# Kernel optimization log

Measured on AMD Instinct MI355X. Metric: run time of the kernel, lower is better.

Reference implementation:

```python
import jax, jax.numpy as jnp
import numpy as np

EPS = 1e-5
EMBED_DIM = 1024
CTX_DIM = 768
NUM_HEADS = 16
DH = EMBED_DIM // NUM_HEADS
# Faithful to torch source: embed_dim // num_heads ** 0.5 parses as embed_dim // (num_heads**0.5)
SCALE = EMBED_DIM // (NUM_HEADS ** 0.5)  # = 256.0


def ws_conv1x1(x, w, b, mask):
    # weight-standardized 1x1 conv1d: w [O, I, 1], x [B, I, T]
    w2 = w[..., 0]
    mu = jnp.mean(w2, axis=1, keepdims=True)
    var = jnp.var(w2, axis=1, keepdims=True)
    wn = (w2 - mu) * jax.lax.rsqrt(var + EPS)
    y = jnp.einsum('oi,bit->bot', wn, x) + b[None, :, None]
    if mask is not None:
        y = jnp.where(mask, y, 0.0)  # mask [B,1,T] bool
    return y


def layernorm(x, g, b):
    # normalize over last axis
    mu = jnp.mean(x, axis=-1, keepdims=True)
    var = jnp.var(x, axis=-1, keepdims=True)
    return (x - mu) * jax.lax.rsqrt(var + EPS) * g + b


def setup_inputs() -> dict:
    key = jax.random.key(0)
    ks = jax.random.split(key, 16)
    B, T, S = 4, 1024, 1024
    inp = {
        'x': jax.random.normal(ks[0], (B, EMBED_DIM, T), dtype=jnp.float32),
        'context': jax.random.normal(ks[1], (B, CTX_DIM, S), dtype=jnp.float32),
        'mask': jax.random.randint(ks[2], (B, 1, T), 0, 2).astype(bool),
        'mask_ctx': jax.random.randint(ks[3], (B, 1, S), 0, 2).astype(bool),
        'qw': jax.random.normal(ks[4], (EMBED_DIM, EMBED_DIM, 1), dtype=jnp.float32) * 0.02,
        'qb': jnp.zeros((EMBED_DIM,), jnp.float32),
        'kw': jax.random.normal(ks[5], (EMBED_DIM, CTX_DIM, 1), dtype=jnp.float32) * 0.02,
        'kb': jnp.zeros((EMBED_DIM,), jnp.float32),
        'vw': jax.random.normal(ks[6], (EMBED_DIM, CTX_DIM, 1), dtype=jnp.float32) * 0.02,
        'vb': jnp.zeros((EMBED_DIM,), jnp.float32),
        'ow': jax.random.normal(ks[7], (EMBED_DIM, EMBED_DIM, 1), dtype=jnp.float32) * 0.02,
        'ob': jnp.zeros((EMBED_DIM,), jnp.float32),
        'gq': jnp.ones((DH,), jnp.float32), 'bq': jnp.zeros((DH,), jnp.float32),
        'gk': jnp.ones((DH,), jnp.float32), 'bk': jnp.zeros((DH,), jnp.float32),
        'gv': jnp.ones((DH,), jnp.float32), 'bv': jnp.zeros((DH,), jnp.float32),
    }
    return inp


def reference(x, context, mask, mask_ctx, qw, qb, kw, kb, vw, vb, ow, ob, gq, bq, gk, bk, gv, bv):
    B, E, T = x.shape
    S = context.shape[-1]
    q = ws_conv1x1(x, qw, qb, mask)            # [B,E,T]
    k = ws_conv1x1(context, kw, kb, mask_ctx)  # [B,E,S]
    v = ws_conv1x1(context, vw, vb, mask_ctx)  # [B,E,S]
    # split heads -> [B,H,dh,L]
    q = q.reshape(B, NUM_HEADS, DH, T)
    k = k.reshape(B, NUM_HEADS, DH, S)
    v = v.reshape(B, NUM_HEADS, DH, S)
    # middle_norm: LayerNorm over dh (applied on transposed layout)
    q = jnp.swapaxes(layernorm(jnp.swapaxes(q, -1, -2), gq, bq), -1, -2)
    k = jnp.swapaxes(layernorm(jnp.swapaxes(k, -1, -2), gk, bk), -1, -2)
    v = jnp.swapaxes(layernorm(jnp.swapaxes(v, -1, -2), gv, bv), -1, -2)
    # scores: k^T @ q -> [B,H,S,T]
    scores = jnp.einsum('bhds,bhdt->bhst', k, q) / SCALE
    scores = jnp.where(mask[:, :, None, :], scores, -1e9)  # mask over query dim T
    scores = jax.nn.softmax(scores, axis=-1)               # softmax over T (as in source)
    scores = jnp.where(mask_ctx[:, :, :, None], scores, 0.0)
    out = jnp.einsum('bhds,bhst->bhdt', v, scores)          # v @ scores -> [B,H,dh,T]
    out = out.reshape(B, E, T)
    out = ws_conv1x1(out, ow, ob, mask) + x
    return out
```

## Files before the change

### kernel.cpp

```cpp
#include <hip/hip_runtime.h>

#define NB 4
#define TT 1024
#define SS 1024
#define EE 1024
#define CCH 768
#define NH 16
#define DHH 64
#define EPSF 1e-5f
#define QSCALE (1.4426950408889634f / 256.0f)

typedef unsigned short u16;
typedef __attribute__((ext_vector_type(8))) short short8;
typedef __attribute__((ext_vector_type(8))) unsigned short u16x8;
typedef __attribute__((ext_vector_type(4))) unsigned short u16x4;
typedef __attribute__((ext_vector_type(4))) float f32x4;

__device__ __forceinline__ u16 f2bu(float f) {
    union { float f; unsigned u; } x; x.f = f;
    unsigned r = x.u + 0x7fffu + ((x.u >> 16) & 1u);
    return (u16)(r >> 16);
}
__device__ __forceinline__ float bu2f(u16 u) {
    union { unsigned u; float f; } x; x.u = ((unsigned)u) << 16; return x.f;
}

#if __has_builtin(__builtin_amdgcn_exp2f)
#define EXP2(x) __builtin_amdgcn_exp2f(x)
#else
#define EXP2(x) exp2f(x)
#endif

#define MFMA16(a, b, c) __builtin_amdgcn_mfma_f32_16x16x32_bf16((a), (b), (c), 0, 0, 0)

__global__ __launch_bounds__(256) void mask_scan(
    const int* __restrict__ mask, const int* __restrict__ mask_ctx,
    int* __restrict__ posQ, int* __restrict__ posK,
    int* __restrict__ tIdx, int* __restrict__ sIdx,
    int* __restrict__ cntQ, int* __restrict__ cntK) {
    int which = blockIdx.x & 1, b = blockIdx.x >> 1;
    const int* m = (which ? mask_ctx : mask) + b * 1024;
    int* pos = (which ? posK : posQ) + b * 1024;
    int* idx = (which ? sIdx : tIdx) + b * 1024;
    int* cnt = (which ? cntK : cntQ) + b;
    int tid = threadIdx.x;
    int base = tid * 4;
    int v[4]; int s = 0;
#pragma unroll
    for (int i = 0; i < 4; i++) { v[i] = m[base + i] ? 1 : 0; s += v[i]; }
    int lane = tid & 63, wid = tid >> 6;
    int inc = s;
#pragma unroll
    for (int off = 1; off < 64; off <<= 1) {
        int o = __shfl_up(inc, off);
        if (lane >= off) inc += o;
    }
    __shared__ int wtot[4];
    if (lane == 63) wtot[wid] = inc;
    __syncthreads();
    int woff = 0;
    for (int i = 0; i < wid; i++) woff += wtot[i];
    int p = woff + inc - s;
#pragma unroll
    for (int i = 0; i < 4; i++) {
        pos[base + i] = p;
        if (v[i]) idx[p] = base + i;
        p += v[i];
    }
    if (tid == 255) *cnt = p;
}

__global__ __launch_bounds__(256) void ws_norm4(
    const float* __restrict__ qw, const float* __restrict__ kw,
    const float* __restrict__ vw, const float* __restrict__ ow,
    u16* __restrict__ wqn, u16* __restrict__ wkn,
    u16* __restrict__ wvn, u16* __restrict__ won) {
    int mat = blockIdx.y;
    const float* w = mat == 0 ? qw : (mat == 1 ? kw : (mat == 2 ? vw : ow));
    u16* wn = mat == 0 ? wqn : (mat == 1 ? wkn : (mat == 2 ? wvn : won));
    int I = (mat == 1 || mat == 2) ? CCH : EE;
    int row = blockIdx.x;
    const float* wr = w + (size_t)row * I;
    float s = 0.f, s2 = 0.f;
    for (int i = threadIdx.x; i < I; i += 256) { float v = wr[i]; s += v; s2 += v * v; }
#pragma unroll
    for (int off = 32; off > 0; off >>= 1) { s += __shfl_down(s, off); s2 += __shfl_down(s2, off); }
    __shared__ float sa[4], sb[4], smean, srstd;
    int wid = threadIdx.x >> 6;
    if ((threadIdx.x & 63) == 0) { sa[wid] = s; sb[wid] = s2; }
    __syncthreads();
    if (threadIdx.x == 0) {
        float ts = sa[0] + sa[1] + sa[2] + sa[3];
        float ts2 = sb[0] + sb[1] + sb[2] + sb[3];
        float mean = ts / (float)I;
        float var = ts2 / (float)I - mean * mean;
        smean = mean; srstd = rsqrtf(var + EPSF);
    }
    __syncthreads();
    float mean = smean, r = srstd;
    u16* wo = wn + (size_t)row * I;
    for (int i = threadIdx.x; i < I; i += 256) wo[i] = f2bu((wr[i] - mean) * r);
}

__global__ __launch_bounds__(256) void transpose2_f2b(
    const float* __restrict__ x, const float* __restrict__ ctx,
    u16* __restrict__ xT, u16* __restrict__ cT) {
    __shared__ float tile[64][65];
    int yy = blockIdx.y;
    int mat = yy < 16 ? 0 : 1;
    int r0 = (mat == 0 ? yy : yy - 16) * 64;
    int R = mat == 0 ? EE : CCH;
    const float* in = mat == 0 ? x : ctx;
    u16* out = mat == 0 ? xT : cT;
    int c0 = blockIdx.x * 64, b = blockIdx.z;
    const float* ip = in + (size_t)b * R * 1024;
    u16* op = out + (size_t)b * R * 1024;
    int tid = threadIdx.x;
#pragma unroll
    for (int m = 0; m < 16; m++) {
        int id = tid + 256 * m; int r = id >> 6, c = id & 63;
        tile[r][c] = ip[(size_t)(r0 + r) * 1024 + c0 + c];
    }
    __syncthreads();
#pragma unroll
    for (int m = 0; m < 16; m++) {
        int id = tid + 256 * m; int rr = id >> 6, cc = id & 63;
        op[(size_t)(c0 + rr) * R + r0 + cc] = f2bu(tile[cc][rr]);
    }
}

__device__ __forceinline__ void gemm_core(
    const u16* __restrict__ A, const u16* __restrict__ Bp, int I,
    int o0, int l0, u16 (*at)[72], u16 (*bt)[72], f32x4 (&acc)[4][2]) {
    int tid = threadIdx.x;
    int w = tid >> 6, lane = tid & 63, quad = lane >> 4, l16 = lane & 15;
    int wm = w & 1, wn = w >> 1;
    int rA = tid >> 3, cA = (tid & 7) * 8;
    u16x8 ra[2][4], rb[2][2];
#pragma unroll
    for (int p = 0; p < 2; p++) {
        int kb = p * 64;
#pragma unroll
        for (int m = 0; m < 4; m++)
            ra[p][m] = *(const u16x8*)&A[(size_t)(o0 + rA + 32 * m) * I + kb + cA];
#pragma unroll
        for (int m = 0; m < 2; m++)
            rb[p][m] = *(const u16x8*)&Bp[(size_t)(l0 + rA + 32 * m) * I + kb + cA];
    }
    for (int k0 = 0; k0 < I; k0 += 128) {
#pragma unroll
        for (int half = 0; half < 2; half++) {
            __syncthreads();
#pragma unroll
            for (int m = 0; m < 4; m++) *(u16x8*)&at[rA + 32 * m][cA] = ra[half][m];
#pragma unroll
            for (int m = 0; m < 2; m++) *(u16x8*)&bt[rA + 32 * m][cA] = rb[half][m];
            __syncthreads();
            int kpre = k0 + half * 64 + 128;
            if (kpre < I) {
#pragma unroll
                for (int m = 0; m < 4; m++)
                    ra[half][m] = *(const u16x8*)&A[(size_t)(o0 + rA + 32 * m) * I + kpre + cA];
#pragma unroll
                for (int m = 0; m < 2; m++)
                    rb[half][m] = *(const u16x8*)&Bp[(size_t)(l0 + rA + 32 * m) * I + kpre + cA];
            }
#pragma unroll
            for (int ks = 0; ks < 64; ks += 32) {
                short8 af[4], bf[2];
#pragma unroll
                for (int i = 0; i < 4; i++)
                    af[i] = *(const short8*)&at[wm * 64 + i * 16 + l16][ks + quad * 8];
#pragma unroll
                for (int j = 0; j < 2; j++)
                    bf[j] = *(const short8*)&bt[wn * 32 + j * 16 + l16][ks + quad * 8];
#pragma unroll
                for (int mt = 0; mt < 4; mt++)
#pragma unroll
                    for (int nt = 0; nt < 2; nt++)
                        acc[mt][nt] = MFMA16(af[mt], bf[nt], acc[mt][nt]);
            }
        }
    }
}

__global__ __launch_bounds__(256) void proj_qkv(
    const u16* __restrict__ wq, const u16* __restrict__ wk, const u16* __restrict__ wv,
    const u16* __restrict__ xT, const u16* __restrict__ cT,
    const float* __restrict__ qb, const float* __restrict__ kb, const float* __restrict__ vbi,
    const int* __restrict__ mask_t, const int* __restrict__ mask_c,
    const int* __restrict__ posQ, const int* __restrict__ posK,
    const float* __restrict__ gq, const float* __restrict__ bq,
    const float* __restrict__ gk, const float* __restrict__ bk,
    u16* __restrict__ qc, u16* __restrict__ kc, u16* __restrict__ yv) {
    __shared__ u16 at[128][72];
    __shared__ u16 bt[64][72];
    __shared__ float sg[64], sbe[64], sbias[128];
    int tid = threadIdx.x;
    int w = tid >> 6, lane = tid & 63, quad = lane >> 4, l16 = lane & 15;
    int wm = w & 1, wn = w >> 1;
    int mat = blockIdx.y >> 3;
    int o0 = (blockIdx.y & 7) * 128;
    int l0 = blockIdx.x * 64;
    int b = blockIdx.z;
    const u16* A = mat == 0 ? wq : (mat == 1 ? wk : wv);
    const u16* BT = mat == 0 ? xT : cT;
    const float* bias = mat == 0 ? qb : (mat == 1 ? kb : vbi);
    const int* maskp = mat == 0 ? mask_t : mask_c;
    int I = mat == 0 ? EE : CCH;
    if (mat < 2 && tid < 64) {
        sg[tid] = (mat == 0 ? gq : gk)[tid];
        sbe[tid] = (mat == 0 ? bq : bk)[tid];
    }
    if (tid < 128) sbias[tid] = bias[o0 + tid];

    f32x4 acc[4][2] = {};
    gemm_core(A, BT + (size_t)b * 1024 * I, I, o0, l0, at, bt, acc);

    const int* mrow = maskp + (size_t)b * 1024;
    if (mat < 2) {
        u16* outT = mat == 0 ? qc : kc;
        const int* posArr = (mat == 0 ? posQ : posK) + (size_t)b * 1024;
        float scale = mat == 0 ? QSCALE : 1.0f;
        int h = (o0 >> 6) + wm;
        int bh = b * NH + h;
#pragma unroll
        for (int nt = 0; nt < 2; nt++) {
            int l = l0 + wn * 32 + nt * 16 + l16;
            int mval = mrow[l];
            float vbuf[16];
            float s = 0.f;
#pragma unroll
            for (int mt = 0; mt < 4; mt++)
#pragma unroll
                for (int reg = 0; reg < 4; reg++) {
                    float v = mval ? (acc[mt][nt][reg] + sbias[wm * 64 + mt * 16 + quad * 4 + reg]) : 0.f;
                    vbuf[mt * 4 + reg] = v; s += v;
                }
            s += __shfl_xor(s, 16); s += __shfl_xor(s, 32);
            float mean = s * (1.f / 64);
            float s2 = 0.f;
#pragma unroll
            for (int i = 0; i < 16; i++) { float dv = vbuf[i] - mean; s2 += dv * dv; }
            s2 += __shfl_xor(s2, 16); s2 += __shfl_xor(s2, 32);
            float r = rsqrtf(s2 * (1.f / 64) + EPSF);
            if (mval) {
                int pos = posArr[l];
                u16* op = outT + ((size_t)bh * 1024 + pos) * 64;
#pragma unroll
                for (int mt = 0; mt < 4; mt++) {
                    u16x4 pk;
#pragma unroll
                    for (int reg = 0; reg < 4; reg++) {
                        int d = mt * 16 + quad * 4 + reg;
                        pk[reg] = f2bu(((vbuf[mt * 4 + reg] - mean) * r * sg[d] + sbe[d]) * scale);
                    }
                    *(u16x4*)&op[mt * 16 + quad * 4] = pk;
                }
            }
        }
    } else {
#pragma unroll
        for (int nt = 0; nt < 2; nt++) {
            int l = l0 + wn * 32 + nt * 16 + l16;
            int mval = mrow[l];
#pragma unroll
            for (int mt = 0; mt < 4; mt++)
#pragma unroll
                for (int reg = 0; reg < 4; reg++) {
                    int o = o0 + wm * 64 + mt * 16 + quad * 4 + reg;
                    float v = mval ? (acc[mt][nt][reg] + sbias[wm * 64 + mt * 16 + quad * 4 + reg]) : 0.f;
                    yv[((size_t)b * EE + o) * 1024 + l] = f2bu(v);
                }
        }
    }
}

__global__ __launch_bounds__(256) void proj_o(
    const u16* __restrict__ won, const u16* __restrict__ aT,
    const float* __restrict__ obi, const int* __restrict__ mask,
    const float* __restrict__ x, float* __restrict__ out) {
    __shared__ u16 at[128][72];
    __shared__ u16 bt[64][72];
    __shared__ float sbias[128];
    int tid = threadIdx.x;
    int w = tid >> 6, lane = tid & 63, quad = lane >> 4, l16 = lane & 15;
    int wm = w & 1, wn = w >> 1;
    int o0 = blockIdx.y * 128, l0 = blockIdx.x * 64, b = blockIdx.z;
    if (tid < 128) sbias[tid] = obi[o0 + tid];
    f32x4 acc[4][2] = {};
    gemm_core(won, aT + (size_t)b * TT * EE, EE, o0, l0, at, bt, acc);
    const int* mrow = mask + (size_t)b * TT;
#pragma unroll
    for (int nt = 0; nt < 2; nt++) {
        int l = l0 + wn * 32 + nt * 16 + l16;
        int mval = mrow[l];
#pragma unroll
        for (int mt = 0; mt < 4; mt++)
#pragma unroll
            for (int reg = 0; reg < 4; reg++) {
                int o = o0 + wm * 64 + mt * 16 + quad * 4 + reg;
                float v = mval ? (acc[mt][nt][reg] + sbias[wm * 64 + mt * 16 + quad * 4 + reg]) : 0.f;
                size_t off = ((size_t)b * EE + o) * TT + l;
                out[off] = v + x[off];
            }
    }
}

__global__ __launch_bounds__(256) void attn_stats_mfma(
    const u16* __restrict__ qc, const u16* __restrict__ kc,
    const int* __restrict__ sIdx, const int* __restrict__ cntQ, const int* __restrict__ cntK,
    const float* __restrict__ gv, const float* __restrict__ bv,
    const u16* __restrict__ yv, u16* __restrict__ vc) {
    int s0 = blockIdx.x * 64, h = blockIdx.y, b = blockIdx.z;
    int Sc = cntK[b], Tc = cntQ[b];
    if (s0 >= Sc) return;
    __shared__ u16 kt[64][72];
    __shared__ u16 qt[64][72];
    __shared__ float lp[4][64];
    int tid = threadIdx.x;
    int w = tid >> 6, lane = tid & 63, quad = lane >> 4, l16 = lane & 15;
    int head = b * NH + h;
    const u16* kp = kc + (size_t)head * SS * DHH;
    const u16* qp = qc + (size_t)head * TT * DHH;
    int rA = tid >> 3, cA = (tid & 7) * 8;
#pragma unroll
    for (int m = 0; m < 2; m++)
        *(u16x8*)&kt[rA + 32 * m][cA] = *(const u16x8*)&kp[(size_t)(s0 + rA + 32 * m) * DHH + cA];
    u16x8 rq[2][2];
#pragma unroll
    for (int p = 0; p < 2; p++)
#pragma unroll
        for (int m = 0; m < 2; m++)
            rq[p][m] = *(const u16x8*)&qp[(size_t)(p * 64 + rA + 32 * m) * DHH + cA];
    float rl[4][4] = {};
    for (int t0 = 0; t0 < Tc; t0 += 128) {
#pragma unroll
        for (int half = 0; half < 2; half++) {
            int tb = t0 + half * 64;
            __syncthreads();
#pragma unroll
            for (int m = 0; m < 2; m++) *(u16x8*)&qt[rA + 32 * m][cA] = rq[half][m];
            __syncthreads();
            int tpre = tb + 128;
            if (tpre < TT) {
#pragma unroll
                for (int m = 0; m < 2; m++)
                    rq[half][m] = *(const u16x8*)&qp[(size_t)(tpre + rA + 32 * m) * DHH + cA];
            }
            int tcol = tb + w * 16 + l16;
            f32x4 acc[4] = {};
#pragma unroll
            for (int ks = 0; ks < 64; ks += 32) {
                short8 bf = *(const short8*)&qt[w * 16 + l16][ks + quad * 8];
#pragma unroll
                for (int mt = 0; mt < 4; mt++) {
                    short8 af = *(const short8*)&kt[mt * 16 + l16][ks + quad * 8];
                    acc[mt] = MFMA16(af, bf, acc[mt]);
                }
            }
            if (tcol < Tc) {
#pragma unroll
                for (int mt = 0; mt < 4; mt++)
#pragma unroll
                    for (int reg = 0; reg < 4; reg++)
                        rl[mt][reg] += EXP2(acc[mt][reg]);
            }
        }
    }
#pragma unroll
    for (int mt = 0; mt < 4; mt++) {
#pragma unroll
        for (int reg = 0; reg < 4; reg++) {
            float v = rl[mt][reg];
            v += __shfl_xor(v, 1); v += __shfl_xor(v, 2);
            v += __shfl_xor(v, 4); v += __shfl_xor(v, 8);
            if (l16 == 0) lp[w][mt * 16 + quad * 4 + reg] = v;
        }
    }
    __syncthreads();
    if (tid < 64 && s0 + tid < Sc) {
        int spos = s0 + tid;
        float lv = lp[0][tid] + lp[1][tid] + lp[2][tid] + lp[3][tid];
        float wsc = lv > 0.f ? (1.f / lv) : 0.f;
        int sreal = sIdx[(size_t)b * 1024 + spos];
        const u16* vin = yv + ((size_t)b * EE + h * 64) * SS + sreal;
        u16* vout = vc + ((size_t)b * EE + h * 64) * SS + spos;
        float sm = 0.f, s2 = 0.f;
        float vals[DHH];
#pragma unroll
        for (int d = 0; d < DHH; d++) {
            float v = bu2f(vin[(size_t)d * SS]);
            vals[d] = v; sm += v; s2 += v * v;
        }
        float mean = sm * (1.f / DHH);
        float var = s2 * (1.f / DHH) - mean * mean;
        float r = rsqrtf(var + EPSF);
#pragma unroll
        for (int d = 0; d < DHH; d++)
            vout[(size_t)d * SS] = f2bu(((vals[d] - mean) * r * gv[d] + bv[d]) * wsc);
    }
}

__global__ __launch_bounds__(256) void attn_pv_mfma(
    const u16* __restrict__ qc, const u16* __restrict__ kc, const u16* __restrict__ vc,
    const int* __restrict__ tIdx, const int* __restrict__ cntQ, const int* __restrict__ cntK,
    u16* __restrict__ aT) {
    int t0 = blockIdx.x * 64, h = blockIdx.y, b = blockIdx.z;
    int Tc = cntQ[b], Sc = cntK[b];
    if (t0 >= Tc) return;
    __shared__ u16 qt[64][72];
    __shared__ u16 kt[64][72];
    __shared__ u16 vt[64][72];
    __shared__ u16 pt[64][72];
    int tid = threadIdx.x;
    int w = tid >> 6, lane = tid & 63, quad = lane >> 4, l16 = lane & 15;
    int head = b * NH + h;
    const u16* qp = qc + (size_t)head * TT * DHH;
    const u16* kp = kc + (size_t)head * SS * DHH;
    const u16* vp = vc + ((size_t)head * DHH) * SS;
    int rA = tid >> 3, cA = (tid & 7) * 8;
#pragma unroll
    for (int m = 0; m < 2; m++)
        *(u16x8*)&qt[rA + 32 * m][cA] = *(const u16x8*)&qp[(size_t)(t0 + rA + 32 * m) * DHH + cA];
    u16x8 rk[2][2], rv[2][2];
#pragma unroll
    for (int p = 0; p < 2; p++)
#pragma unroll
        for (int m = 0; m < 2; m++) {
            rk[p][m] = *(const u16x8*)&kp[(size_t)(p * 64 + rA + 32 * m) * DHH + cA];
            rv[p][m] = *(const u16x8*)&vp[(size_t)(rA + 32 * m) * SS + p * 64 + cA];
        }
    int tl = w * 16 + l16;

    f32x4 oacc[4] = {};
    for (int s0 = 0; s0 < Sc; s0 += 128) {
#pragma unroll
        for (int half = 0; half < 2; half++) {
            int sb = s0 + half * 64;
            if (sb >= Sc) break;
            __syncthreads();
#pragma unroll
            for (int m = 0; m < 2; m++) {
                *(u16x8*)&kt[rA + 32 * m][cA] = rk[half][m];
                *(u16x8*)&vt[rA + 32 * m][cA] = rv[half][m];
            }
            __syncthreads();
            int spre = sb + 128;
            if (spre < SS) {
#pragma unroll
                for (int m = 0; m < 2; m++) {
                    rk[half][m] = *(const u16x8*)&kp[(size_t)(spre + rA + 32 * m) * DHH + cA];
                    rv[half][m] = *(const u16x8*)&vp[(size_t)(rA + 32 * m) * SS + spre + cA];
                }
            }
            f32x4 acc[4] = {};
#pragma unroll
            for (int ks = 0; ks < 64; ks += 32) {
                short8 bf = *(const short8*)&qt[tl][ks + quad * 8];
#pragma unroll
                for (int mt = 0; mt < 4; mt++) {
                    short8 af = *(const short8*)&kt[mt * 16 + l16][ks + quad * 8];
                    acc[mt] = MFMA16(af, bf, acc[mt]);
                }
            }
#pragma unroll
            for (int mt = 0; mt < 4; mt++) {
                u16x4 pk;
#pragma unroll
                for (int reg = 0; reg < 4; reg++) {
                    int sl = mt * 16 + quad * 4 + reg;
                    pk[reg] = (sb + sl < Sc) ? f2bu(EXP2(acc[mt][reg])) : (u16)0;
                }
                *(u16x4*)&pt[tl][mt * 16 + quad * 4] = pk;
            }
#pragma unroll
            for (int ks = 0; ks < 64; ks += 32) {
                short8 bf = *(const short8*)&pt[tl][ks + quad * 8];
#pragma unroll
                for (int mt = 0; mt < 4; mt++) {
                    short8 af = *(const short8*)&vt[mt * 16 + l16][ks + quad * 8];
                    oacc[mt] = MFMA16(af, bf, oacc[mt]);
                }
            }
        }
    }
    __syncthreads();
#pragma unroll
    for (int mt = 0; mt < 4; mt++) {
        u16x4 pk;
#pragma unroll
        for (int reg = 0; reg < 4; reg++) pk[reg] = f2bu(oacc[mt][reg]);
        *(u16x4*)&pt[tl][mt * 16 + quad * 4] = pk;
    }
    __syncthreads();
    const int* ti = tIdx + (size_t)b * 1024;
#pragma unroll
    for (int i = 0; i < 2; i++) {
        int id = tid * 2 + i;
        int r = id >> 3, c = (id & 7) * 8;
        if (t0 + r < Tc) {
            int treal = ti[t0 + r];
            *(u16x8*)&aT[((size_t)b * TT + treal) * EE + h * 64 + c] =
                *(const u16x8*)&pt[r][c];
        }
    }
}

extern "C" void kernel_launch(void* const* d_in, const int* in_sizes, int n_in,
                              void* d_out, int out_size, void* d_ws, size_t ws_size,
                              hipStream_t stream) {
    const float* x        = (const float*)d_in[0];
    const float* ctx      = (const float*)d_in[1];
    const int*   mask     = (const int*)d_in[2];
    const int*   mask_ctx = (const int*)d_in[3];
    const float* qw  = (const float*)d_in[4];
    const float* qbi = (const float*)d_in[5];
    const float* kw  = (const float*)d_in[6];
    const float* kbi = (const float*)d_in[7];
    const float* vw  = (const float*)d_in[8];
    const float* vbi = (const float*)d_in[9];
    const float* ow  = (const float*)d_in[10];
    const float* obi = (const float*)d_in[11];
    const float* gq = (const float*)d_in[12];
    const float* bq = (const float*)d_in[13];
    const float* gk = (const float*)d_in[14];
    const float* bk = (const float*)d_in[15];
    const float* gv = (const float*)d_in[16];
    const float* bv = (const float*)d_in[17];

    u16* p = (u16*)d_ws;
    u16* wqn = p; p += (size_t)EE * EE;
    u16* wkn = p; p += (size_t)EE * CCH;
    u16* wvn = p; p += (size_t)EE * CCH;
    u16* won = p; p += (size_t)EE * EE;
    u16* xT  = p; p += (size_t)NB * TT * EE;
    u16* cT  = p; p += (size_t)NB * SS * CCH;
    u16* yv  = p; p += (size_t)NB * EE * SS;
    u16* qc  = p; p += (size_t)NB * NH * TT * DHH;
    u16* kc  = p; p += (size_t)NB * NH * SS * DHH;
    u16* vc  = p; p += (size_t)NB * EE * SS;
    u16* aT  = p; p += (size_t)NB * TT * EE;
    int* posQ = (int*)p;
    int* posK = posQ + NB * 1024;
    int* tIdx = posK + NB * 1024;
    int* sIdx = tIdx + NB * 1024;
    int* cntQ = sIdx + NB * 1024;
    int* cntK = cntQ + NB;

    mask_scan<<<8, 256, 0, stream>>>(mask, mask_ctx, posQ, posK, tIdx, sIdx, cntQ, cntK);

    ws_norm4<<<dim3(1024, 4), 256, 0, stream>>>(qw, kw, vw, ow, wqn, wkn, wvn, won);

    transpose2_f2b<<<dim3(16, 28, NB), 256, 0, stream>>>(x, ctx, xT, cT);

    proj_qkv<<<dim3(16, 24, NB), 256, 0, stream>>>(
        wqn, wkn, wvn, xT, cT, qbi, kbi, vbi, mask, mask_ctx, posQ, posK,
        gq, bq, gk, bk, qc, kc, yv);

    attn_stats_mfma<<<dim3(16, NH, NB), 256, 0, stream>>>(
        qc, kc, sIdx, cntQ, cntK, gv, bv, yv, vc);

    attn_pv_mfma<<<dim3(16, NH, NB), 256, 0, stream>>>(
        qc, kc, vc, tIdx, cntQ, cntK, aT);

    proj_o<<<dim3(16, 8, NB), 256, 0, stream>>>(won, aT, obi, mask, x, (float*)d_out);
}
```

Baseline: 236.0 us.

## Compact masked tokens before QKV projection and skip fully masked GEMM tiles

The transpose kernel now runs its own prefix scan over the mask and writes only unmasked tokens, packed, into the bf16 transposed inputs. The QKV projection then exits early for tiles past the valid count, so it does roughly half the GEMM work. The separate mask-scan kernel is merged into the weight-standardization launch as an extra grid row, removing one launch. The trade-off is a redundant scan in every transpose block. Rows of the compacted buffers beyond the valid count are left unwritten, and downstream kernels are assumed to ignore them.

```diff
diff --git a/kernel.cpp b/kernel.cpp
--- a/kernel.cpp
+++ b/kernel.cpp
@@ -33,48 +33,46 @@
 
 #define MFMA16(a, b, c) __builtin_amdgcn_mfma_f32_16x16x32_bf16((a), (b), (c), 0, 0, 0)
 
-__global__ __launch_bounds__(256) void mask_scan(
-    const int* __restrict__ mask, const int* __restrict__ mask_ctx,
-    int* __restrict__ posQ, int* __restrict__ posK,
-    int* __restrict__ tIdx, int* __restrict__ sIdx,
-    int* __restrict__ cntQ, int* __restrict__ cntK) {
-    int which = blockIdx.x & 1, b = blockIdx.x >> 1;
-    const int* m = (which ? mask_ctx : mask) + b * 1024;
-    int* pos = (which ? posK : posQ) + b * 1024;
-    int* idx = (which ? sIdx : tIdx) + b * 1024;
-    int* cnt = (which ? cntK : cntQ) + b;
-    int tid = threadIdx.x;
-    int base = tid * 4;
-    int v[4]; int s = 0;
-#pragma unroll
-    for (int i = 0; i < 4; i++) { v[i] = m[base + i] ? 1 : 0; s += v[i]; }
-    int lane = tid & 63, wid = tid >> 6;
-    int inc = s;
-#pragma unroll
-    for (int off = 1; off < 64; off <<= 1) {
-        int o = __shfl_up(inc, off);
-        if (lane >= off) inc += o;
-    }
-    __shared__ int wtot[4];
-    if (lane == 63) wtot[wid] = inc;
-    __syncthreads();
-    int woff = 0;
-    for (int i = 0; i < wid; i++) woff += wtot[i];
-    int p = woff + inc - s;
-#pragma unroll
-    for (int i = 0; i < 4; i++) {
-        pos[base + i] = p;
-        if (v[i]) idx[p] = base + i;
-        p += v[i];
-    }
-    if (tid == 255) *cnt = p;
-}
-
-__global__ __launch_bounds__(256) void ws_norm4(
+__global__ __launch_bounds__(256) void ws_norm_scan(
     const float* __restrict__ qw, const float* __restrict__ kw,
     const float* __restrict__ vw, const float* __restrict__ ow,
     u16* __restrict__ wqn, u16* __restrict__ wkn,
-    u16* __restrict__ wvn, u16* __restrict__ won) {
+    u16* __restrict__ wvn, u16* __restrict__ won,
+    const int* __restrict__ mask, const int* __restrict__ mask_ctx,
+    int* __restrict__ tIdx, int* __restrict__ sIdx,
+    int* __restrict__ cntQ, int* __restrict__ cntK) {
+    int tid = threadIdx.x;
+    if (blockIdx.y == 4) {
+        if (blockIdx.x >= 8) return;
+        int which = blockIdx.x & 1, b = blockIdx.x >> 1;
+        const int* m = (which ? mask_ctx : mask) + b * 1024;
+        int* idx = (which ? sIdx : tIdx) + b * 1024;
+        int* cnt = (which ? cntK : cntQ) + b;
+        int base = tid * 4;
+        int v[4]; int s = 0;
+#pragma unroll
+        for (int i = 0; i < 4; i++) { v[i] = m[base + i] ? 1 : 0; s += v[i]; }
+        int lane = tid & 63, wid = tid >> 6;
+        int inc = s;
+#pragma unroll
+        for (int off = 1; off < 64; off <<= 1) {
+            int o = __shfl_up(inc, off);
+            if (lane >= off) inc += o;
+        }
+        __shared__ int wtot[4];
+        if (lane == 63) wtot[wid] = inc;
+        __syncthreads();
+        int woff = 0;
+        for (int i = 0; i < wid; i++) woff += wtot[i];
+        int p = woff + inc - s;
+#pragma unroll
+        for (int i = 0; i < 4; i++) {
+            if (v[i]) idx[p] = base + i;
+            p += v[i];
+        }
+        if (tid == 255) *cnt = p;
+        return;
+    }
     int mat = blockIdx.y;
     const float* w = mat == 0 ? qw : (mat == 1 ? kw : (mat == 2 ? vw : ow));
     u16* wn = mat == 0 ? wqn : (mat == 1 ? wkn : (mat == 2 ? wvn : won));
@@ -82,14 +80,14 @@
     int row = blockIdx.x;
     const float* wr = w + (size_t)row * I;
     float s = 0.f, s2 = 0.f;
-    for (int i = threadIdx.x; i < I; i += 256) { float v = wr[i]; s += v; s2 += v * v; }
+    for (int i = tid; i < I; i += 256) { float v = wr[i]; s += v; s2 += v * v; }
 #pragma unroll
     for (int off = 32; off > 0; off >>= 1) { s += __shfl_down(s, off); s2 += __shfl_down(s2, off); }
     __shared__ float sa[4], sb[4], smean, srstd;
-    int wid = threadIdx.x >> 6;
-    if ((threadIdx.x & 63) == 0) { sa[wid] = s; sb[wid] = s2; }
-    __syncthreads();
-    if (threadIdx.x == 0) {
+    int wid = tid >> 6;
+    if ((tid & 63) == 0) { sa[wid] = s; sb[wid] = s2; }
+    __syncthreads();
+    if (tid == 0) {
         float ts = sa[0] + sa[1] + sa[2] + sa[3];
         float ts2 = sb[0] + sb[1] + sb[2] + sb[3];
         float mean = ts / (float)I;
@@ -99,33 +97,59 @@
     __syncthreads();
     float mean = smean, r = srstd;
     u16* wo = wn + (size_t)row * I;
-    for (int i = threadIdx.x; i < I; i += 256) wo[i] = f2bu((wr[i] - mean) * r);
-}
-
-__global__ __launch_bounds__(256) void transpose2_f2b(
+    for (int i = tid; i < I; i += 256) wo[i] = f2bu((wr[i] - mean) * r);
+}
+
+__global__ __launch_bounds__(256) void transpose2_compact(
     const float* __restrict__ x, const float* __restrict__ ctx,
-    u16* __restrict__ xT, u16* __restrict__ cT) {
+    const int* __restrict__ mask, const int* __restrict__ mask_ctx,
+    u16* __restrict__ xc, u16* __restrict__ cc) {
     __shared__ float tile[64][65];
+    __shared__ int spos[64], smask[64], wtot[4];
     int yy = blockIdx.y;
     int mat = yy < 16 ? 0 : 1;
     int r0 = (mat == 0 ? yy : yy - 16) * 64;
     int R = mat == 0 ? EE : CCH;
     const float* in = mat == 0 ? x : ctx;
-    u16* out = mat == 0 ? xT : cT;
+    const int* m = (mat == 0 ? mask : mask_ctx) + (size_t)blockIdx.z * 1024;
+    u16* out = mat == 0 ? xc : cc;
     int c0 = blockIdx.x * 64, b = blockIdx.z;
     const float* ip = in + (size_t)b * R * 1024;
     u16* op = out + (size_t)b * R * 1024;
     int tid = threadIdx.x;
 #pragma unroll
-    for (int m = 0; m < 16; m++) {
-        int id = tid + 256 * m; int r = id >> 6, c = id & 63;
+    for (int mm = 0; mm < 16; mm++) {
+        int id = tid + 256 * mm; int r = id >> 6, c = id & 63;
         tile[r][c] = ip[(size_t)(r0 + r) * 1024 + c0 + c];
     }
-    __syncthreads();
-#pragma unroll
-    for (int m = 0; m < 16; m++) {
-        int id = tid + 256 * m; int rr = id >> 6, cc = id & 63;
-        op[(size_t)(c0 + rr) * R + r0 + cc] = f2bu(tile[cc][rr]);
+    int base = tid * 4;
+    int v[4]; int s = 0;
+#pragma unroll
+    for (int i = 0; i < 4; i++) { v[i] = m[base + i] ? 1 : 0; s += v[i]; }
+    int lane = tid & 63, wid = tid >> 6;
+    int inc = s;
+#pragma unroll
+    for (int off = 1; off < 64; off <<= 1) {
+        int o = __shfl_up(inc, off);
+        if (lane >= off) inc += o;
+    }
+    if (lane == 63) wtot[wid] = inc;
+    __syncthreads();
+    int woff = 0;
+    for (int i = 0; i < wid; i++) woff += wtot[i];
+    int p = woff + inc - s;
+#pragma unroll
+    for (int i = 0; i < 4; i++) {
+        int g = base + i;
+        if (g >= c0 && g < c0 + 64) { spos[g - c0] = p; smask[g - c0] = v[i]; }
+        p += v[i];
+    }
+    __syncthreads();
+#pragma unroll
+    for (int mm = 0; mm < 16; mm++) {
+        int id = tid + 256 * mm; int rr = id >> 6, cc2 = id & 63;
+        if (smask[rr])
+            op[(size_t)spos[rr] * R + r0 + cc2] = f2bu(tile[cc2][rr]);
     }
 }
 
@@ -186,27 +210,27 @@
 
 __global__ __launch_bounds__(256) void proj_qkv(
     const u16* __restrict__ wq, const u16* __restrict__ wk, const u16* __restrict__ wv,
-    const u16* __restrict__ xT, const u16* __restrict__ cT,
+    const u16* __restrict__ xc, const u16* __restrict__ cc,
     const float* __restrict__ qb, const float* __restrict__ kb, const float* __restrict__ vbi,
-    const int* __restrict__ mask_t, const int* __restrict__ mask_c,
-    const int* __restrict__ posQ, const int* __restrict__ posK,
+    const int* __restrict__ cntQ, const int* __restrict__ cntK,
     const float* __restrict__ gq, const float* __restrict__ bq,
     const float* __restrict__ gk, const float* __restrict__ bk,
     u16* __restrict__ qc, u16* __restrict__ kc, u16* __restrict__ yv) {
+    int mat = blockIdx.y >> 3;
+    int l0 = blockIdx.x * 64;
+    int b = blockIdx.z;
+    int limit = (mat == 0) ? cntQ[b] : cntK[b];
+    if (l0 >= limit) return;
     __shared__ u16 at[128][72];
     __shared__ u16 bt[64][72];
     __shared__ float sg[64], sbe[64], sbias[128];
     int tid = threadIdx.x;
     int w = tid >> 6, lane = tid & 63, quad = lane >> 4, l16 = lane & 15;
     int wm = w & 1, wn = w >> 1;
-    int mat = blockIdx.y >> 3;
     int o0 = (blockIdx.y & 7) * 128;
-    int l0 = blockIdx.x * 64;
-    int b = blockIdx.z;
     const u16* A = mat == 0 ? wq : (mat == 1 ? wk : wv);
-    const u16* BT = mat == 0 ? xT : cT;
+    const u16* BT = mat == 0 ? xc : cc;
     const float* bias = mat == 0 ? qb : (mat == 1 ? kb : vbi);
-    const int* maskp = mat == 0 ? mask_t : mask_c;
     int I = mat == 0 ? EE : CCH;
     if (mat < 2 && tid < 64) {
         sg[tid] = (mat == 0 ? gq : gk)[tid];
@@ -217,24 +241,21 @@
     f32x4 acc[4][2] = {};
     gemm_core(A, BT + (size_t)b * 1024 * I, I, o0, l0, at, bt, acc);
 
-    const int* mrow = maskp + (size_t)b * 1024;
     if (mat < 2) {
         u16* outT = mat == 0 ? qc : kc;
-        const int* posArr = (mat == 0 ? posQ : posK) + (size_t)b * 1024;
         float scale = mat == 0 ? QSCALE : 1.0f;
         int h = (o0 >> 6) + wm;
         int bh = b * NH + h;
 #pragma unroll
         for (int nt = 0; nt < 2; nt++) {
             int l = l0 + wn * 32 + nt * 16 + l16;
-            int mval = mrow[l];
             float vbuf[16];
             float s = 0.f;
 #pragma unroll
             for (int mt = 0; mt < 4; mt++)
 #pragma unroll
                 for (int reg = 0; reg < 4; reg++) {
-                    float v = mval ? (acc[mt][nt][reg] + sbias[wm * 64 + mt * 16 + quad * 4 + reg]) : 0.f;
+                    float v = acc[mt][nt][reg] + sbias[wm * 64 + mt * 16 + quad * 4 + reg];
                     vbuf[mt * 4 + reg] = v; s += v;
                 }
             s += __shfl_xor(s, 16); s += __shfl_xor(s, 32);
@@ -244,9 +265,8 @@
             for (int i = 0; i < 16; i++) { float dv = vbuf[i] - mean; s2 += dv * dv; }
             s2 += __shfl_xor(s2, 16); s2 += __shfl_xor(s2, 32);
             float r = rsqrtf(s2 * (1.f / 64) + EPSF);
-            if (mval) {
-                int pos = posArr[l];
-                u16* op = outT + ((size_t)bh * 1024 + pos) * 64;
+            if (l < limit) {
+                u16* op = outT + ((size_t)bh * 1024 + l) * 64;
 #pragma unroll
                 for (int mt = 0; mt < 4; mt++) {
                     u16x4 pk;
@@ -263,15 +283,16 @@
 #pragma unroll
         for (int nt = 0; nt < 2; nt++) {
             int l = l0 + wn * 32 + nt * 16 + l16;
-            int mval = mrow[l];
-#pragma unroll
-            for (int mt = 0; mt < 4; mt++)
-#pragma unroll
-                for (int reg = 0; reg < 4; reg++) {
-                    int o = o0 + wm * 64 + mt * 16 + quad * 4 + reg;
-                    float v = mval ? (acc[mt][nt][reg] + sbias[wm * 64 + mt * 16 + quad * 4 + reg]) : 0.f;
-                    yv[((size_t)b * EE + o) * 1024 + l] = f2bu(v);
-                }
+            if (l < limit) {
+#pragma unroll
+                for (int mt = 0; mt < 4; mt++)
+#pragma unroll
+                    for (int reg = 0; reg < 4; reg++) {
+                        int o = o0 + wm * 64 + mt * 16 + quad * 4 + reg;
+                        float v = acc[mt][nt][reg] + sbias[wm * 64 + mt * 16 + quad * 4 + reg];
+                        yv[((size_t)b * EE + o) * 1024 + l] = f2bu(v);
+                    }
+            }
         }
     }
 }
@@ -309,7 +330,7 @@
 
 __global__ __launch_bounds__(256) void attn_stats_mfma(
     const u16* __restrict__ qc, const u16* __restrict__ kc,
-    const int* __restrict__ sIdx, const int* __restrict__ cntQ, const int* __restrict__ cntK,
+    const int* __restrict__ cntQ, const int* __restrict__ cntK,
     const float* __restrict__ gv, const float* __restrict__ bv,
     const u16* __restrict__ yv, u16* __restrict__ vc) {
     int s0 = blockIdx.x * 64, h = blockIdx.y, b = blockIdx.z;
@@ -383,8 +404,7 @@
         int spos = s0 + tid;
         float lv = lp[0][tid] + lp[1][tid] + lp[2][tid] + lp[3][tid];
         float wsc = lv > 0.f ? (1.f / lv) : 0.f;
-        int sreal = sIdx[(size_t)b * 1024 + spos];
-        const u16* vin = yv + ((size_t)b * EE + h * 64) * SS + sreal;
+        const u16* vin = yv + ((size_t)b * EE + h * 64) * SS + spos;
         u16* vout = vc + ((size_t)b * EE + h * 64) * SS + spos;
         float sm = 0.f, s2 = 0.f;
         float vals[DHH];
@@ -534,32 +554,30 @@
     u16* wkn = p; p += (size_t)EE * CCH;
     u16* wvn = p; p += (size_t)EE * CCH;
     u16* won = p; p += (size_t)EE * EE;
-    u16* xT  = p; p += (size_t)NB * TT * EE;
-    u16* cT  = p; p += (size_t)NB * SS * CCH;
+    u16* xc  = p; p += (size_t)NB * TT * EE;
+    u16* cc  = p; p += (size_t)NB * SS * CCH;
     u16* yv  = p; p += (size_t)NB * EE * SS;
     u16* qc  = p; p += (size_t)NB * NH * TT * DHH;
     u16* kc  = p; p += (size_t)NB * NH * SS * DHH;
     u16* vc  = p; p += (size_t)NB * EE * SS;
     u16* aT  = p; p += (size_t)NB * TT * EE;
-    int* posQ = (int*)p;
-    int* posK = posQ + NB * 1024;
-    int* tIdx = posK + NB * 1024;
+    int* tIdx = (int*)p;
     int* sIdx = tIdx + NB * 1024;
     int* cntQ = sIdx + NB * 1024;
     int* cntK = cntQ + NB;
 
-    mask_scan<<<8, 256, 0, stream>>>(mask, mask_ctx, posQ, posK, tIdx, sIdx, cntQ, cntK);
-
-    ws_norm4<<<dim3(1024, 4), 256, 0, stream>>>(qw, kw, vw, ow, wqn, wkn, wvn, won);
-
-    transpose2_f2b<<<dim3(16, 28, NB), 256, 0, stream>>>(x, ctx, xT, cT);
+    ws_norm_scan<<<dim3(1024, 5), 256, 0, stream>>>(
+        qw, kw, vw, ow, wqn, wkn, wvn, won, mask, mask_ctx, tIdx, sIdx, cntQ, cntK);
+
+    transpose2_compact<<<dim3(16, 28, NB), 256, 0, stream>>>(
+        x, ctx, mask, mask_ctx, xc, cc);
 
     proj_qkv<<<dim3(16, 24, NB), 256, 0, stream>>>(
-        wqn, wkn, wvn, xT, cT, qbi, kbi, vbi, mask, mask_ctx, posQ, posK,
+        wqn, wkn, wvn, xc, cc, qbi, kbi, vbi, cntQ, cntK,
         gq, bq, gk, bk, qc, kc, yv);
 
     attn_stats_mfma<<<dim3(16, NH, NB), 256, 0, stream>>>(
-        qc, kc, sIdx, cntQ, cntK, gv, bv, yv, vc);
+        qc, kc, cntQ, cntK, gv, bv, yv, vc);
 
     attn_pv_mfma<<<dim3(16, NH, NB), 256, 0, stream>>>(
         qc, kc, vc, tIdx, cntQ, cntK, aT);
```

After: 232.7 us. Within noise of the previous version (-1.4%).
